# Kernel tuning notes

Measured on AMD Instinct MI355X. Metric: run time of the kernel, lower is better.

Reference implementation:

```python
import jax, jax.numpy as jnp
import numpy as np

N_NODES = 50000
N_EDGES = 800000
IN_CH = 128
HID = 64   # 2 * out_channels
OUT = 32   # out_channels
SLOPE = 0.2  # PyG GATConv default negative_slope


def _gat_layer(x, W, a_src, a_dst, b, src, dst):
    """Single-head GATConv: proj -> edge attention logits -> segment softmax
    over destination nodes -> scatter-aggregate weighted source messages."""
    n = x.shape[0]
    h = x @ W                                   # [N, C]
    ls = h @ a_src                              # [N] per-node src score
    ld = h @ a_dst                              # [N] per-node dst score
    logits = jax.nn.leaky_relu(ls[src] + ld[dst], negative_slope=SLOPE)  # [E]
    # numerically stable segment softmax grouped by destination node
    lmax = jax.ops.segment_max(logits, dst, num_segments=n)              # [N]
    e = jnp.exp(logits - lmax[dst])                                      # [E]
    denom = jax.ops.segment_sum(e, dst, num_segments=n)                  # [N]
    alpha = e / denom[dst]                                               # [E]
    out = jax.ops.segment_sum(alpha[:, None] * h[src], dst, num_segments=n)
    return out + b


def setup_inputs() -> dict:
    key = jax.random.key(0)
    ks = jax.random.split(key, 10)
    x = jax.random.normal(ks[0], (N_NODES, IN_CH), dtype=jnp.float32)
    edge_index = jax.random.randint(ks[1], (2, N_EDGES), 0, N_NODES, dtype=jnp.int32)
    s1 = 1.0 / np.sqrt(IN_CH)
    s2 = 1.0 / np.sqrt(HID)
    return {
        "x": x,
        "edge_index": edge_index,
        "W1": jax.random.normal(ks[2], (IN_CH, HID), dtype=jnp.float32) * s1,
        "a_src1": jax.random.normal(ks[3], (HID,), dtype=jnp.float32) * s2,
        "a_dst1": jax.random.normal(ks[4], (HID,), dtype=jnp.float32) * s2,
        "b1": jnp.zeros((HID,), dtype=jnp.float32),
        "W2": jax.random.normal(ks[5], (HID, OUT), dtype=jnp.float32) * s2,
        "a_src2": jax.random.normal(ks[6], (OUT,), dtype=jnp.float32) / np.sqrt(OUT),
        "a_dst2": jax.random.normal(ks[7], (OUT,), dtype=jnp.float32) / np.sqrt(OUT),
        "b2": jnp.zeros((OUT,), dtype=jnp.float32),
    }


def reference(x, edge_index, W1, a_src1, a_dst1, b1, W2, a_src2, a_dst2, b2):
    src, dst = edge_index[0], edge_index[1]
    h = jax.nn.relu(_gat_layer(x, W1, a_src1, a_dst1, b1, src, dst))
    return _gat_layer(h, W2, a_src2, a_dst2, b2, src, dst)
```

## Files before the change

kernel.cpp:

```cpp
#include <hip/hip_runtime.h>
#include <hip/hip_fp16.h>


#define N_NODES 50000
#define N_EDGES 800000
#define SLOPE 0.2f
#define NBUCK 196
#define CAP 4608
#define BIN_BLOCKS 196
#define GEMM_BLOCKS 782

typedef _Float16 half4 __attribute__((ext_vector_type(4)));

__global__ __launch_bounds__(256) void k_zerobins(int* __restrict__ binctr)
{
    if (threadIdx.x < NBUCK) binctr[threadIdx.x] = 0;
}

__global__ __launch_bounds__(256) void k_pre(
    const int* __restrict__ src, const int* __restrict__ dst,
    int* __restrict__ binctr, int* __restrict__ stg,
    const float* __restrict__ x, const float* __restrict__ W1,
    const float* __restrict__ a_src, const float* __restrict__ a_dst,
    _Float16* __restrict__ h1h, float* __restrict__ ls, float* __restrict__ ld)
{
    __shared__ float As[64][128];
    __shared__ float Bs[128][64];
    __shared__ int hist[NBUCK];
    __shared__ int gb[NBUCK];
    const int tid = threadIdx.x;

    if (blockIdx.x < BIN_BLOCKS) {
        if (tid < NBUCK) hist[tid] = 0;
        __syncthreads();

        const int base = blockIdx.x * 4096;
        int ms[16], md[16], mr[16];
        #pragma unroll
        for (int k = 0; k < 16; ++k) {
            int e = base + tid + k * 256;
            int s = 0, d = 0;
            if (e < N_EDGES) { s = src[e]; d = dst[e]; }
            ms[k] = s; md[k] = d;
            mr[k] = (e < N_EDGES) ? atomicAdd(&hist[d >> 8], 1) : -1;
        }
        __syncthreads();
        if (tid < NBUCK) gb[tid] = atomicAdd(&binctr[tid], hist[tid]);
        __syncthreads();
        #pragma unroll
        for (int k = 0; k < 16; ++k) {
            if (mr[k] >= 0) {
                int b = md[k] >> 8;
                stg[b * CAP + gb[b] + mr[k]] = ms[k] | ((md[k] & 255) << 16);
            }
        }
        return;
    }

    const int m0 = (blockIdx.x - BIN_BLOCKS) * 64;

    {
        const float4* Wv = (const float4*)W1;
        float4* Bv = (float4*)&Bs[0][0];
        #pragma unroll
        for (int i = 0; i < 8; ++i) Bv[tid + i * 256] = Wv[tid + i * 256];
    }
    {
        const float4* Xv = (const float4*)x;
        #pragma unroll
        for (int i = 0; i < 8; ++i) {
            int idx = tid + i * 256;
            int r = idx >> 5, kq = idx & 31;
            float4 v = make_float4(0.f, 0.f, 0.f, 0.f);
            if (m0 + r < N_NODES) v = Xv[(size_t)(m0 + r) * 32 + kq];
            ((float4*)&As[r][0])[kq] = v;
        }
    }
    __syncthreads();

    const int tx = tid & 15, ty = tid >> 4;
    const int c0 = tx * 4, r0 = ty * 4;
    float acc[4][4] = {};
    for (int k = 0; k < 128; k += 4) {
        float a_s[4][4];
        #pragma unroll
        for (int i = 0; i < 4; ++i) {
            float4 av = *(const float4*)&As[r0 + i][k];
            a_s[i][0] = av.x; a_s[i][1] = av.y; a_s[i][2] = av.z; a_s[i][3] = av.w;
        }
        #pragma unroll
        for (int kk = 0; kk < 4; ++kk) {
            float4 b = *(const float4*)&Bs[k + kk][c0];
            #pragma unroll
            for (int i = 0; i < 4; ++i) {
                acc[i][0] += a_s[i][kk] * b.x;
                acc[i][1] += a_s[i][kk] * b.y;
                acc[i][2] += a_s[i][kk] * b.z;
                acc[i][3] += a_s[i][kk] * b.w;
            }
        }
    }

    float as4[4], ad4[4];
    #pragma unroll
    for (int j = 0; j < 4; ++j) { as4[j] = a_src[c0 + j]; ad4[j] = a_dst[c0 + j]; }

    #pragma unroll
    for (int i = 0; i < 4; ++i) {
        int row = m0 + r0 + i;
        float pls = acc[i][0]*as4[0] + acc[i][1]*as4[1] + acc[i][2]*as4[2] + acc[i][3]*as4[3];
        float pld = acc[i][0]*ad4[0] + acc[i][1]*ad4[1] + acc[i][2]*ad4[2] + acc[i][3]*ad4[3];
        #pragma unroll
        for (int off = 1; off < 16; off <<= 1) {
            pls += __shfl_xor(pls, off, 64);
            pld += __shfl_xor(pld, off, 64);
        }
        if (row < N_NODES) {
            half4 hv;
            hv.x = (_Float16)acc[i][0]; hv.y = (_Float16)acc[i][1];
            hv.z = (_Float16)acc[i][2]; hv.w = (_Float16)acc[i][3];
            ((half4*)&h1h[(size_t)row * 64])[tx] = hv;
            if (tx == 0) { ls[row] = pls; ld[row] = pld; }
        }
    }
}

__global__ __launch_bounds__(1024) void k_sort(
    const int* __restrict__ stg, const int* __restrict__ binctr,
    int* __restrict__ row_start, unsigned short* __restrict__ csr_src)
{
    __shared__ int cnt[256];
    __shared__ int off[256];
    __shared__ int sc[256];
    const int b = blockIdx.x, t = threadIdx.x;
    const int n = binctr[b];
    const int sbase = b * CAP;

    if (t < 256) { sc[t] = (t < NBUCK) ? binctr[t] : 0; cnt[t] = 0; }
    __syncthreads();
    #pragma unroll
    for (int o = 1; o < 256; o <<= 1) {
        int u = (t < 256 && t >= o) ? sc[t - o] : 0;
        __syncthreads();
        if (t < 256) sc[t] += u;
        __syncthreads();
    }
    const int obase = sc[b] - n;

    int mv[5], mk[5], mr[5];
    int c = 0;
    for (int i = t; i < n; i += 1024) {
        int v = stg[sbase + i];
        int k = v >> 16;
        mv[c] = v & 0xFFFF;
        mk[c] = k;
        mr[c] = atomicAdd(&cnt[k], 1);
        ++c;
    }
    __syncthreads();

    if (t < 256) off[t] = cnt[t];
    __syncthreads();
    #pragma unroll
    for (int o = 1; o < 256; o <<= 1) {
        int u = (t < 256 && t >= o) ? off[t - o] : 0;
        __syncthreads();
        if (t < 256) off[t] += u;
        __syncthreads();
    }

    if (t < 256) {
        int node = b * 256 + t;
        if (node < N_NODES) row_start[node] = obase + off[t] - cnt[t];
    }
    if (b == NBUCK - 1 && t == 0) row_start[N_NODES] = N_EDGES;

    for (int i = 0; i < c; ++i)
        csr_src[obase + off[mk[i]] - cnt[mk[i]] + mr[i]] = (unsigned short)mv[i];
}

__global__ __launch_bounds__(256) void k_agg1(
    const unsigned short* __restrict__ csr_src, const int* __restrict__ row_start,
    const float* __restrict__ ls, const float* __restrict__ ld,
    const _Float16* __restrict__ h1h, const float* __restrict__ b1,
    float* __restrict__ acc1)
{
    const int node = blockIdx.x * 4 + (threadIdx.x >> 6);
    const int lane = threadIdx.x & 63;
    const int c4 = lane & 15, eslot = lane >> 4;
    const int beg = row_start[node], end = row_start[node + 1];
    const float ldv = ld[node];
    const half4* H = (const half4*)h1h;

    float4 acc = make_float4(0.f, 0.f, 0.f, 0.f);
    float sw = 0.f;
    for (int base = beg; base < end; base += 64) {
        const int cnt = min(64, end - base);
        int s = 0;
        float w = 0.f;
        if (lane < cnt) {
            s = csr_src[base + lane];
            float l = ls[s] + ldv;
            l = l > 0.f ? l : SLOPE * l;
            w = __expf(l);
        }
        float wsum = w;
        #pragma unroll
        for (int off = 1; off < 64; off <<= 1) wsum += __shfl_xor(wsum, off, 64);
        sw += wsum;

        int j = 0;
        for (; j + 8 <= cnt; j += 8) {
            int   s0 = __shfl(s, j + eslot, 64);
            int   s1 = __shfl(s, j + 4 + eslot, 64);
            float w0 = __shfl(w, j + eslot, 64);
            float w1 = __shfl(w, j + 4 + eslot, 64);
            half4 g0 = H[(size_t)s0 * 16 + c4];
            half4 g1 = H[(size_t)s1 * 16 + c4];
            acc.x += w0 * (float)g0.x; acc.y += w0 * (float)g0.y;
            acc.z += w0 * (float)g0.z; acc.w += w0 * (float)g0.w;
            acc.x += w1 * (float)g1.x; acc.y += w1 * (float)g1.y;
            acc.z += w1 * (float)g1.z; acc.w += w1 * (float)g1.w;
        }
        for (; j < cnt; j += 4) {
            int   sj = __shfl(s, j + eslot, 64);
            float wj = __shfl(w, j + eslot, 64);
            half4 g = H[(size_t)sj * 16 + c4];
            acc.x += wj * (float)g.x; acc.y += wj * (float)g.y;
            acc.z += wj * (float)g.z; acc.w += wj * (float)g.w;
        }
    }
    #pragma unroll
    for (int off = 16; off < 64; off <<= 1) {
        acc.x += __shfl_xor(acc.x, off, 64);
        acc.y += __shfl_xor(acc.y, off, 64);
        acc.z += __shfl_xor(acc.z, off, 64);
        acc.w += __shfl_xor(acc.w, off, 64);
    }
    if (eslot == 0) {
        float inv = sw > 0.f ? 1.f / sw : 0.f;
        float4 bb = ((const float4*)b1)[c4];
        ((float4*)&acc1[(size_t)node * 64])[c4] =
            make_float4(acc.x * inv + bb.x, acc.y * inv + bb.y,
                        acc.z * inv + bb.z, acc.w * inv + bb.w);
    }
}

__global__ __launch_bounds__(256) void k_epi1(
    const float* __restrict__ acc1, const float* __restrict__ W2,
    const float* __restrict__ a_src2, const float* __restrict__ a_dst2,
    _Float16* __restrict__ h2h, float* __restrict__ ls2, float* __restrict__ ld2)
{
    __shared__ float Hs[64][68];
    __shared__ float W2s[64][32];
    const int tid = threadIdx.x;
    const int n0 = blockIdx.x * 64;

    {
        const float4* Wv = (const float4*)W2;
        float4* Ws = (float4*)&W2s[0][0];
        Ws[tid] = Wv[tid];
        Ws[tid + 256] = Wv[tid + 256];
    }
    {
        const float4* Av = (const float4*)acc1;
        #pragma unroll
        for (int i = 0; i < 4; ++i) {
            int idx = tid + i * 256;
            int r = idx >> 4, kq = idx & 15;
            float4 v = make_float4(0.f, 0.f, 0.f, 0.f);
            if (n0 + r < N_NODES) {
                v = Av[(size_t)(n0 + r) * 16 + kq];
                v.x = fmaxf(v.x, 0.f); v.y = fmaxf(v.y, 0.f);
                v.z = fmaxf(v.z, 0.f); v.w = fmaxf(v.w, 0.f);
            }
            ((float4*)&Hs[r][0])[kq] = v;
        }
    }
    __syncthreads();

    const int nl = tid >> 2, cg = tid & 3, c0 = cg * 8;
    float acc[8] = {};
    for (int k4 = 0; k4 < 16; ++k4) {
        float4 hv4 = *(const float4*)&Hs[nl][k4 * 4];
        #pragma unroll
        for (int kk = 0; kk < 4; ++kk) {
            float hv = kk == 0 ? hv4.x : kk == 1 ? hv4.y : kk == 2 ? hv4.z : hv4.w;
            int k = k4 * 4 + kk;
            float4 w0 = *(const float4*)&W2s[k][c0];
            float4 w1 = *(const float4*)&W2s[k][c0 + 4];
            acc[0] += hv * w0.x; acc[1] += hv * w0.y;
            acc[2] += hv * w0.z; acc[3] += hv * w0.w;
            acc[4] += hv * w1.x; acc[5] += hv * w1.y;
            acc[6] += hv * w1.z; acc[7] += hv * w1.w;
        }
    }

    float pls = 0.f, pld = 0.f;
    #pragma unroll
    for (int j = 0; j < 8; ++j) {
        pls += acc[j] * a_src2[c0 + j];
        pld += acc[j] * a_dst2[c0 + j];
    }
    pls += __shfl_xor(pls, 1, 64); pls += __shfl_xor(pls, 2, 64);
    pld += __shfl_xor(pld, 1, 64); pld += __shfl_xor(pld, 2, 64);

    int node = n0 + nl;
    if (node < N_NODES) {
        half4 lo, hi;
        lo.x = (_Float16)acc[0]; lo.y = (_Float16)acc[1];
        lo.z = (_Float16)acc[2]; lo.w = (_Float16)acc[3];
        hi.x = (_Float16)acc[4]; hi.y = (_Float16)acc[5];
        hi.z = (_Float16)acc[6]; hi.w = (_Float16)acc[7];
        ((half4*)&h2h[(size_t)node * 32])[cg * 2]     = lo;
        ((half4*)&h2h[(size_t)node * 32])[cg * 2 + 1] = hi;
        if (cg == 0) { ls2[node] = pls; ld2[node] = pld; }
    }
}

__global__ __launch_bounds__(256) void k_agg2(
    const unsigned short* __restrict__ csr_src, const int* __restrict__ row_start,
    const float* __restrict__ ls, const float* __restrict__ ld,
    const _Float16* __restrict__ h2h, const float* __restrict__ b2,
    float* __restrict__ out)
{
    const int idx = blockIdx.x * 256 + threadIdx.x;
    const int node = idx >> 5;
    const int grp = idx & 31;
    const int c4 = grp & 7, eslot = grp >> 3;
    const int beg = row_start[node], end = row_start[node + 1];
    const float ldv = ld[node];
    const half4* H = (const half4*)h2h;

    float4 acc = make_float4(0.f, 0.f, 0.f, 0.f);
    float sw = 0.f;
    for (int base = beg; base < end; base += 32) {
        const int cnt = min(32, end - base);
        int s = 0;
        float w = 0.f;
        if (grp < cnt) {
            s = csr_src[base + grp];
            float l = ls[s] + ldv;
            l = l > 0.f ? l : SLOPE * l;
            w = __expf(l);
        }
        float wsum = w;
        #pragma unroll
        for (int off = 1; off < 32; off <<= 1) wsum += __shfl_xor(wsum, off, 32);
        sw += wsum;

        int j = 0;
        for (; j + 8 <= cnt; j += 8) {
            int   s0 = __shfl(s, j + eslot, 32);
            int   s1 = __shfl(s, j + 4 + eslot, 32);
            float w0 = __shfl(w, j + eslot, 32);
            float w1 = __shfl(w, j + 4 + eslot, 32);
            half4 g0 = H[(size_t)s0 * 8 + c4];
            half4 g1 = H[(size_t)s1 * 8 + c4];
            acc.x += w0 * (float)g0.x; acc.y += w0 * (float)g0.y;
            acc.z += w0 * (float)g0.z; acc.w += w0 * (float)g0.w;
            acc.x += w1 * (float)g1.x; acc.y += w1 * (float)g1.y;
            acc.z += w1 * (float)g1.z; acc.w += w1 * (float)g1.w;
        }
        for (; j < cnt; j += 4) {
            int   sj = __shfl(s, j + eslot, 32);
            float wj = __shfl(w, j + eslot, 32);
            half4 g = H[(size_t)sj * 8 + c4];
            acc.x += wj * (float)g.x; acc.y += wj * (float)g.y;
            acc.z += wj * (float)g.z; acc.w += wj * (float)g.w;
        }
    }
    #pragma unroll
    for (int off = 8; off < 32; off <<= 1) {
        acc.x += __shfl_xor(acc.x, off, 32);
        acc.y += __shfl_xor(acc.y, off, 32);
        acc.z += __shfl_xor(acc.z, off, 32);
        acc.w += __shfl_xor(acc.w, off, 32);
    }
    if (eslot == 0) {
        float inv = sw > 0.f ? 1.f / sw : 0.f;
        float4 bb = ((const float4*)b2)[c4];
        ((float4*)&out[(size_t)node * 32])[c4] =
            make_float4(acc.x * inv + bb.x, acc.y * inv + bb.y,
                        acc.z * inv + bb.z, acc.w * inv + bb.w);
    }
}

extern "C" void kernel_launch(void* const* d_in, const int* in_sizes, int n_in,
                              void* d_out, int out_size, void* d_ws, size_t ws_size,
                              hipStream_t stream)
{
    const float* x      = (const float*)d_in[0];
    const int*   ei     = (const int*)  d_in[1];
    const float* W1     = (const float*)d_in[2];
    const float* a_src1 = (const float*)d_in[3];
    const float* a_dst1 = (const float*)d_in[4];
    const float* b1     = (const float*)d_in[5];
    const float* W2     = (const float*)d_in[6];
    const float* a_src2 = (const float*)d_in[7];
    const float* a_dst2 = (const float*)d_in[8];
    const float* b2     = (const float*)d_in[9];
    const int* src = ei;
    const int* dst = ei + N_EDGES;
    float* out = (float*)d_out;

    float* ws   = (float*)d_ws;
    _Float16* h1h = (_Float16*)ws;
    float* acc1 = ws + 1600000;
    float* ls1  = ws + 4800000;
    float* ld1  = ws + 4850000;
    int* row_start = (int*)(ws + 4900000);
    unsigned short* csr16 = (unsigned short*)(ws + 4950016);
    int* binctr = (int*)(ws + 5350032);
    int* stg    = (int*)(ws + 5350288);
    _Float16* h2h = h1h;
    float* ls2 = ls1;
    float* ld2 = ld1;

    k_zerobins<<<1, 256, 0, stream>>>(binctr);
    k_pre  <<<BIN_BLOCKS + GEMM_BLOCKS, 256, 0, stream>>>(
        src, dst, binctr, stg, x, W1, a_src1, a_dst1, h1h, ls1, ld1);
    k_sort <<<NBUCK, 1024, 0, stream>>>(stg, binctr, row_start, csr16);
    k_agg1 <<<12500, 256, 0, stream>>>(csr16, row_start, ls1, ld1, h1h, b1, acc1);
    k_epi1 <<<782,  256, 0, stream>>>(acc1, W2, a_src2, a_dst2, h2h, ls2, ld2);
    k_agg2 <<<6250, 256, 0, stream>>>(csr16, row_start, ls2, ld2, h2h, b2, out);
}
```

Baseline: 169.5 us.

## Fuse layer-2 projection and attention scores into layer-1 aggregation kernel

Merges the layer-1 aggregation kernel with the epilogue that applied ReLU, multiplied by W2 and computed layer-2 source and destination scores. Each wavefront now applies bias and ReLU to its aggregated row, spreads the row with shuffles, and does the 64x32 matvec against W2 held in shared memory. This removes one kernel launch and the fp32 acc1 round trip through global memory. In exchange, every block loads W2 into LDS and the matvec uses many cross-lane shuffles. The workspace layout is repacked so h2h, ls2 and ld2 get their own buffers and no longer alias the layer-1 ones.

```diff
diff --git a/kernel.cpp b/kernel.cpp
--- a/kernel.cpp
+++ b/kernel.cpp
@@ -179,14 +179,26 @@
         csr_src[obase + off[mk[i]] - cnt[mk[i]] + mr[i]] = (unsigned short)mv[i];
 }
 
-__global__ __launch_bounds__(256) void k_agg1(
+__global__ __launch_bounds__(256) void k_agg1f(
     const unsigned short* __restrict__ csr_src, const int* __restrict__ row_start,
     const float* __restrict__ ls, const float* __restrict__ ld,
     const _Float16* __restrict__ h1h, const float* __restrict__ b1,
-    float* __restrict__ acc1)
-{
-    const int node = blockIdx.x * 4 + (threadIdx.x >> 6);
-    const int lane = threadIdx.x & 63;
+    const float* __restrict__ W2,
+    const float* __restrict__ a_src2, const float* __restrict__ a_dst2,
+    _Float16* __restrict__ h2h, float* __restrict__ ls2, float* __restrict__ ld2)
+{
+    __shared__ float W2s[64][32];
+    const int tid = threadIdx.x;
+    {
+        const float4* Wv = (const float4*)W2;
+        float4* Ws = (float4*)&W2s[0][0];
+        Ws[tid] = Wv[tid];
+        Ws[tid + 256] = Wv[tid + 256];
+    }
+    __syncthreads();
+
+    const int node = blockIdx.x * 4 + (tid >> 6);
+    const int lane = tid & 63;
     const int c4 = lane & 15, eslot = lane >> 4;
     const int beg = row_start[node], end = row_start[node + 1];
     const float ldv = ld[node];
@@ -237,85 +249,41 @@
         acc.z += __shfl_xor(acc.z, off, 64);
         acc.w += __shfl_xor(acc.w, off, 64);
     }
-    if (eslot == 0) {
-        float inv = sw > 0.f ? 1.f / sw : 0.f;
-        float4 bb = ((const float4*)b1)[c4];
-        ((float4*)&acc1[(size_t)node * 64])[c4] =
-            make_float4(acc.x * inv + bb.x, acc.y * inv + bb.y,
-                        acc.z * inv + bb.z, acc.w * inv + bb.w);
-    }
-}
-
-__global__ __launch_bounds__(256) void k_epi1(
-    const float* __restrict__ acc1, const float* __restrict__ W2,
-    const float* __restrict__ a_src2, const float* __restrict__ a_dst2,
-    _Float16* __restrict__ h2h, float* __restrict__ ls2, float* __restrict__ ld2)
-{
-    __shared__ float Hs[64][68];
-    __shared__ float W2s[64][32];
-    const int tid = threadIdx.x;
-    const int n0 = blockIdx.x * 64;
-
-    {
-        const float4* Wv = (const float4*)W2;
-        float4* Ws = (float4*)&W2s[0][0];
-        Ws[tid] = Wv[tid];
-        Ws[tid + 256] = Wv[tid + 256];
-    }
-    {
-        const float4* Av = (const float4*)acc1;
-        #pragma unroll
-        for (int i = 0; i < 4; ++i) {
-            int idx = tid + i * 256;
-            int r = idx >> 4, kq = idx & 15;
-            float4 v = make_float4(0.f, 0.f, 0.f, 0.f);
-            if (n0 + r < N_NODES) {
-                v = Av[(size_t)(n0 + r) * 16 + kq];
-                v.x = fmaxf(v.x, 0.f); v.y = fmaxf(v.y, 0.f);
-                v.z = fmaxf(v.z, 0.f); v.w = fmaxf(v.w, 0.f);
-            }
-            ((float4*)&Hs[r][0])[kq] = v;
-        }
-    }
-    __syncthreads();
-
-    const int nl = tid >> 2, cg = tid & 3, c0 = cg * 8;
-    float acc[8] = {};
-    for (int k4 = 0; k4 < 16; ++k4) {
-        float4 hv4 = *(const float4*)&Hs[nl][k4 * 4];
-        #pragma unroll
-        for (int kk = 0; kk < 4; ++kk) {
-            float hv = kk == 0 ? hv4.x : kk == 1 ? hv4.y : kk == 2 ? hv4.z : hv4.w;
-            int k = k4 * 4 + kk;
-            float4 w0 = *(const float4*)&W2s[k][c0];
-            float4 w1 = *(const float4*)&W2s[k][c0 + 4];
-            acc[0] += hv * w0.x; acc[1] += hv * w0.y;
-            acc[2] += hv * w0.z; acc[3] += hv * w0.w;
-            acc[4] += hv * w1.x; acc[5] += hv * w1.y;
-            acc[6] += hv * w1.z; acc[7] += hv * w1.w;
-        }
-    }
-
-    float pls = 0.f, pld = 0.f;
-    #pragma unroll
-    for (int j = 0; j < 8; ++j) {
-        pls += acc[j] * a_src2[c0 + j];
-        pld += acc[j] * a_dst2[c0 + j];
-    }
-    pls += __shfl_xor(pls, 1, 64); pls += __shfl_xor(pls, 2, 64);
-    pld += __shfl_xor(pld, 1, 64); pld += __shfl_xor(pld, 2, 64);
-
-    int node = n0 + nl;
-    if (node < N_NODES) {
-        half4 lo, hi;
-        lo.x = (_Float16)acc[0]; lo.y = (_Float16)acc[1];
-        lo.z = (_Float16)acc[2]; lo.w = (_Float16)acc[3];
-        hi.x = (_Float16)acc[4]; hi.y = (_Float16)acc[5];
-        hi.z = (_Float16)acc[6]; hi.w = (_Float16)acc[7];
-        ((half4*)&h2h[(size_t)node * 32])[cg * 2]     = lo;
-        ((half4*)&h2h[(size_t)node * 32])[cg * 2 + 1] = hi;
-        if (cg == 0) { ls2[node] = pls; ld2[node] = pld; }
-    }
+
+    const float inv = sw > 0.f ? 1.f / sw : 0.f;
+    const float4 bb = ((const float4*)b1)[c4];
+    float4 r;
+    r.x = fmaxf(acc.x * inv + bb.x, 0.f);
+    r.y = fmaxf(acc.y * inv + bb.y, 0.f);
+    r.z = fmaxf(acc.z * inv + bb.z, 0.f);
+    r.w = fmaxf(acc.w * inv + bb.w, 0.f);
+
+    const int kh = lane >> 5, ch = lane & 31;
+    float hv = 0.f;
+    #pragma unroll
+    for (int jj = 0; jj < 32; jj += 4) {
+        int holder = 8 * kh + (jj >> 2);
+        float r0 = __shfl(r.x, holder, 64);
+        float r1 = __shfl(r.y, holder, 64);
+        float r2 = __shfl(r.z, holder, 64);
+        float r3 = __shfl(r.w, holder, 64);
+        int k = 32 * kh + jj;
+        hv += r0 * W2s[k][ch];
+        hv += r1 * W2s[k + 1][ch];
+        hv += r2 * W2s[k + 2][ch];
+        hv += r3 * W2s[k + 3][ch];
+    }
+    hv += __shfl_xor(hv, 32, 64);
+
+    float pls = hv * a_src2[ch];
+    float pld = hv * a_dst2[ch];
+    #pragma unroll
+    for (int off = 1; off < 32; off <<= 1) {
+        pls += __shfl_xor(pls, off, 64);
+        pld += __shfl_xor(pld, off, 64);
+    }
+    if (lane < 32) h2h[(size_t)node * 32 + ch] = (_Float16)hv;
+    if (lane == 0) { ls2[node] = pls; ld2[node] = pld; }
 }
 
 __global__ __launch_bounds__(256) void k_agg2(
@@ -406,22 +374,21 @@
 
     float* ws   = (float*)d_ws;
     _Float16* h1h = (_Float16*)ws;
-    float* acc1 = ws + 1600000;
-    float* ls1  = ws + 4800000;
-    float* ld1  = ws + 4850000;
-    int* row_start = (int*)(ws + 4900000);
-    unsigned short* csr16 = (unsigned short*)(ws + 4950016);
-    int* binctr = (int*)(ws + 5350032);
-    int* stg    = (int*)(ws + 5350288);
-    _Float16* h2h = h1h;
-    float* ls2 = ls1;
-    float* ld2 = ld1;
+    _Float16* h2h = (_Float16*)(ws + 1600000);
+    float* ls1  = ws + 2400000;
+    float* ld1  = ws + 2450000;
+    float* ls2  = ws + 2500000;
+    float* ld2  = ws + 2550000;
+    int* row_start = (int*)(ws + 2600000);
+    unsigned short* csr16 = (unsigned short*)(ws + 2650016);
+    int* binctr = (int*)(ws + 3050032);
+    int* stg    = (int*)(ws + 3050288);
 
     k_zerobins<<<1, 256, 0, stream>>>(binctr);
-    k_pre  <<<BIN_BLOCKS + GEMM_BLOCKS, 256, 0, stream>>>(
+    k_pre   <<<BIN_BLOCKS + GEMM_BLOCKS, 256, 0, stream>>>(
         src, dst, binctr, stg, x, W1, a_src1, a_dst1, h1h, ls1, ld1);
-    k_sort <<<NBUCK, 1024, 0, stream>>>(stg, binctr, row_start, csr16);
-    k_agg1 <<<12500, 256, 0, stream>>>(csr16, row_start, ls1, ld1, h1h, b1, acc1);
-    k_epi1 <<<782,  256, 0, stream>>>(acc1, W2, a_src2, a_dst2, h2h, ls2, ld2);
-    k_agg2 <<<6250, 256, 0, stream>>>(csr16, row_start, ls2, ld2, h2h, b2, out);
-}
+    k_sort  <<<NBUCK, 1024, 0, stream>>>(stg, binctr, row_start, csr16);
+    k_agg1f <<<12500, 256, 0, stream>>>(csr16, row_start, ls1, ld1, h1h, b1,
+                                        W2, a_src2, a_dst2, h2h, ls2, ld2);
+    k_agg2  <<<6250, 256, 0, stream>>>(csr16, row_start, ls2, ld2, h2h, b2, out);
+}
```

Measured after the change: 183.5 us. 1.08x slower.
